# Kernel tuning notes

Hardware: AMD Instinct MI355X
Metric: run time of the kernel (lower is better)

Reference implementation:

```python
import jax, jax.numpy as jnp
import numpy as np

B, N_VIS, NUM_PATCHES = 8, 256, 1024
D_MODEL, PATCH = 512, 16
NUM_LAYERS, D_STATE, D_CONV, EXPAND = 4, 16, 4, 2
D_INNER = EXPAND * D_MODEL
DT_RANK = D_MODEL // 16  # ceil(d_model/16) = 32, standard Mamba
EPS = 1e-6


def setup_inputs() -> dict:
    key = jax.random.key(0)
    ks = jax.random.split(key, 20)
    s = 0.02
    inp = {
        "x_visible": jax.random.normal(ks[0], (B, N_VIS, D_MODEL), jnp.float32),
        "ids_visible": jnp.sort(jax.random.randint(ks[1], (B, N_VIS), 0, NUM_PATCHES), axis=-1),
        "mask_token": s * jax.random.normal(ks[2], (1, 1, D_MODEL), jnp.float32),
        "pos_embed": s * jax.random.normal(ks[3], (1, NUM_PATCHES, D_MODEL), jnp.float32),
        "in_proj_w": s * jax.random.normal(ks[4], (NUM_LAYERS, D_MODEL, 2 * D_INNER), jnp.float32),
        "conv_w": s * jax.random.normal(ks[5], (NUM_LAYERS, D_INNER, D_CONV), jnp.float32),
        "conv_b": jnp.zeros((NUM_LAYERS, D_INNER), jnp.float32),
        "x_proj_w": s * jax.random.normal(ks[6], (NUM_LAYERS, D_INNER, DT_RANK + 2 * D_STATE), jnp.float32),
        "dt_proj_w": s * jax.random.normal(ks[7], (NUM_LAYERS, DT_RANK, D_INNER), jnp.float32),
        "dt_proj_b": 0.1 * jax.random.uniform(ks[8], (NUM_LAYERS, D_INNER), jnp.float32),
        "A_log": jnp.broadcast_to(jnp.log(jnp.arange(1, D_STATE + 1, dtype=jnp.float32)), (NUM_LAYERS, D_INNER, D_STATE)) * jnp.ones((NUM_LAYERS, D_INNER, 1)),
        "D_skip": jnp.ones((NUM_LAYERS, D_INNER), jnp.float32),
        "out_proj_w": s * jax.random.normal(ks[9], (NUM_LAYERS, D_INNER, D_MODEL), jnp.float32),
        "block_norm_w": jnp.ones((NUM_LAYERS, D_MODEL), jnp.float32),
        "norm_w": jnp.ones((D_MODEL,), jnp.float32),
        "head_w": s * jax.random.normal(ks[10], (D_MODEL, PATCH), jnp.float32),
        "head_b": jnp.zeros((PATCH,), jnp.float32),
    }
    return inp


def rmsnorm(x, w):
    return x * jax.lax.rsqrt(jnp.mean(x * x, axis=-1, keepdims=True) + EPS) * w


def mamba_block(x, in_w, cw, cb, xp_w, dt_w, dt_b, a_log, d_skip, out_w):
    # x: [B, L, d_model]
    u, z = jnp.split(x @ in_w, 2, axis=-1)  # each [B, L, d_inner]
    # causal depthwise conv1d over L
    u_t = jnp.swapaxes(u, 1, 2)  # [B, d_inner, L]
    u_c = jax.lax.conv_general_dilated(
        u_t, cw[:, None, :], (1,), [(D_CONV - 1, 0)],
        dimension_numbers=("NCH", "OIH", "NCH"), feature_group_count=D_INNER)
    u = jax.nn.silu(jnp.swapaxes(u_c, 1, 2) + cb)  # [B, L, d_inner]
    x_dbl = u @ xp_w  # [B, L, dt_rank + 2*d_state]
    dt, Bm, Cm = jnp.split(x_dbl, [DT_RANK, DT_RANK + D_STATE], axis=-1)
    dt = jax.nn.softplus(dt @ dt_w + dt_b)  # [B, L, d_inner]
    A = -jnp.exp(a_log)  # [d_inner, d_state]

    def step(h, inp):
        dt_t, B_t, C_t, u_tt = inp  # [B,di], [B,ds], [B,ds], [B,di]
        dA = jnp.exp(dt_t[:, :, None] * A)  # [B, di, ds]
        h = dA * h + (dt_t * u_tt)[:, :, None] * B_t[:, None, :]
        y = jnp.einsum("bds,bs->bd", h, C_t)
        return h, y

    bsz = u.shape[0]
    h0 = jnp.zeros((bsz, D_INNER, D_STATE), x.dtype)
    xs = (jnp.swapaxes(dt, 0, 1), jnp.swapaxes(Bm, 0, 1),
          jnp.swapaxes(Cm, 0, 1), jnp.swapaxes(u, 0, 1))
    _, ys = jax.lax.scan(step, h0, xs)  # ys: [L, B, d_inner]
    y = jnp.swapaxes(ys, 0, 1) + u * d_skip
    y = y * jax.nn.silu(z)
    return y @ out_w


def reference(x_visible, ids_visible, mask_token, pos_embed, in_proj_w, conv_w,
              conv_b, x_proj_w, dt_proj_w, dt_proj_b, A_log, D_skip, out_proj_w,
              block_norm_w, norm_w, head_w, head_b):
    bsz = x_visible.shape[0]
    # scatter visible tokens into full mask-token canvas
    x_full = jnp.broadcast_to(mask_token, (bsz, NUM_PATCHES, D_MODEL))
    b_idx = jnp.arange(bsz)[:, None]
    x_full = x_full.at[b_idx, ids_visible].set(x_visible)
    x = x_full + pos_embed
    for i in range(NUM_LAYERS):
        x = x + mamba_block(rmsnorm(x, block_norm_w[i]), in_proj_w[i], conv_w[i],
                            conv_b[i], x_proj_w[i], dt_proj_w[i], dt_proj_b[i],
                            A_log[i], D_skip[i], out_proj_w[i])
    x = rmsnorm(x, norm_w)
    return x @ head_w + head_b
```

## Files before the change

### kernel.cpp

```cpp
#include <hip/hip_runtime.h>

typedef unsigned short u16;
typedef unsigned int   u32;
typedef __attribute__((ext_vector_type(8))) short bf16x8;
typedef __attribute__((ext_vector_type(4))) float f32x4;

__device__ __forceinline__ float b2f(u16 u) {
    union { u32 i; float f; } v; v.i = ((u32)u) << 16; return v.f;
}
__device__ __forceinline__ u16 f2b(float f) {
    union { float f; u32 i; } v; v.f = f;
    u32 x = v.i;
    return (u16)((x + 0x7fffu + ((x >> 16) & 1u)) >> 16);
}
__device__ __forceinline__ float ldf(const void* p, size_t i, int bf) {
    return bf ? b2f(((const u16*)p)[i]) : ((const float*)p)[i];
}

__global__ __launch_bounds__(256)
void prep_k(const void* __restrict__ alog, const void* __restrict__ dsk,
            const void* __restrict__ normw,
            float* __restrict__ a2f, float* __restrict__ df,
            int* __restrict__ flag)
{
    const int bf = (((const u16*)normw)[0] == 0x3F80u) ? 1 : 0;
    const int t = blockIdx.x * 256 + threadIdx.x;
    if (t == 0) { flag[0] = bf; flag[1] = 1; }
    const float v = -expf(ldf(alog, t, bf)) * 1.44269504f;
    a2f[t] = v;
    const float base = -expf(ldf(alog, t & ~15, bf)) * 1.44269504f;
    const float expect = (float)((t & 15) + 1) * base;
    if (fabsf(v - expect) > 1e-4f * fabsf(expect) + 1e-7f)
        atomicAnd(&flag[1], 0);
    if (t < 4096) df[t] = ldf(dsk, t, bf);
}

template<int BM, int EPI>
__global__ __launch_bounds__(256)
void gemm_gld_k(const u16* __restrict__ A, int lda,
                const u16* __restrict__ Bt, int K,
                float* __restrict__ C, int ldc,
                u16* __restrict__ C2)
{
    __shared__ __align__(16) u16 As[BM * 64];
    __shared__ __align__(16) u16 Bs[128 * 64];

    const int tid = threadIdx.x;
    const int NX = gridDim.x, NY = gridDim.y;
    const int bid = blockIdx.y * NX + blockIdx.x;
    const int xcd = bid & 7, j = bid >> 3;
    const int m_idx = xcd * (NY >> 3) + j / NX;
    const int n_idx = j % NX;
    const int m0 = m_idx * BM, n0 = n_idx * 128;

    const int lane = tid & 63, wave = tid >> 6;
    const int wr = wave >> 1, wc = wave & 1;
    constexpr int WM = BM / 2, FM = WM / 16;
    constexpr int AJ = BM / 32;

    const int lr = lane >> 3;
    const int skc = (lane & 7) ^ lr;

    f32x4 acc[FM][4] = {};

    for (int k0 = 0; k0 < K; k0 += 64) {
        #pragma unroll
        for (int j2 = 0; j2 < AJ; ++j2) {
            const int R = wave * (BM / 4) + j2 * 8;
            __builtin_amdgcn_global_load_lds(
                (const u32*)&A[(size_t)(m0 + R + lr) * lda + k0 + skc * 8],
                (u32*)&As[R * 64], 16, 0, 0);
        }
        #pragma unroll
        for (int j2 = 0; j2 < 4; ++j2) {
            const int R = wave * 32 + j2 * 8;
            __builtin_amdgcn_global_load_lds(
                (const u32*)&Bt[(size_t)(n0 + R + lr) * K + k0 + skc * 8],
                (u32*)&Bs[R * 64], 16, 0, 0);
        }
        __syncthreads();
        #pragma unroll
        for (int ks = 0; ks < 2; ++ks) {
            bf16x8 af[FM], bfr[4];
            const int chunk = ((ks * 4 + (lane >> 4)) ^ (lane & 7)) * 8;
            #pragma unroll
            for (int fm = 0; fm < FM; ++fm) {
                int m = wr * WM + fm * 16 + (lane & 15);
                af[fm] = *reinterpret_cast<const bf16x8*>(&As[m * 64 + chunk]);
            }
            #pragma unroll
            for (int fn = 0; fn < 4; ++fn) {
                int n = wc * 64 + fn * 16 + (lane & 15);
                bfr[fn] = *reinterpret_cast<const bf16x8*>(&Bs[n * 64 + chunk]);
            }
            #pragma unroll
            for (int fm = 0; fm < FM; ++fm)
                #pragma unroll
                for (int fn = 0; fn < 4; ++fn)
                    acc[fm][fn] = __builtin_amdgcn_mfma_f32_16x16x32_bf16(
                        af[fm], bfr[fn], acc[fm][fn], 0, 0, 0);
        }
        __syncthreads();
    }

    #pragma unroll
    for (int fm = 0; fm < FM; ++fm) {
        #pragma unroll
        for (int fn = 0; fn < 4; ++fn) {
            #pragma unroll
            for (int r = 0; r < 4; ++r) {
                int row = m0 + wr * WM + fm * 16 + ((lane >> 4) << 2) + r;
                int col = n0 + wc * 64 + fn * 16 + (lane & 15);
                float v = acc[fm][fn][r];
                size_t ci = (size_t)row * ldc + col;
                if constexpr (EPI == 0) C2[ci] = f2b(v);
                else                    C[ci] += v;
            }
        }
    }
}

template<int BM, int BN, int BK, int EPI, int SPLITK = 1, int AF32 = 0>
__global__ __launch_bounds__(256)
void gemm_k(const u16* __restrict__ A, int lda,
            const u16* __restrict__ Bt, int K,
            float* __restrict__ C, int ldc,
            u16* __restrict__ C2,
            const void* __restrict__ bias, int boff, const int* __restrict__ bff,
            int sstride = 0)
{
    constexpr int PAD = 8;
    constexpr int LDS_S = BK + PAD;
    __shared__ __align__(16) u16 As[BM * LDS_S];
    __shared__ __align__(16) u16 Bs[BN * LDS_S];

    const int tid = threadIdx.x;
    const int m0 = blockIdx.y * BM;
    int n0, kbeg, kend;
    if constexpr (SPLITK > 1) {
        n0 = 0;
        const int ksz = K / SPLITK;
        kbeg = blockIdx.x * ksz;
        kend = kbeg + ksz;
        C += (size_t)blockIdx.x * sstride;
    } else {
        n0 = blockIdx.x * BN;
        kbeg = 0; kend = K;
    }
    const int lane = tid & 63, wv = tid >> 6;
    const int wr = wv >> 1, wc = wv & 1;
    constexpr int WM = BM / 2, WN = BN / 2, FM = WM / 16, FN = WN / 16;
    constexpr int AC = (BM * BK) / 2048;
    constexpr int BC = (BN * BK) / 2048;
    constexpr int KC = BK / 8;

    f32x4 acc[FM][FN] = {};

    for (int k0 = kbeg; k0 < kend; k0 += BK) {
        #pragma unroll
        for (int i = 0; i < AC; ++i) {
            int idx = tid + i * 256;
            int row = idx / KC, kc = idx % KC;
            if constexpr (AF32) {
                const float* Af = (const float*)A;
                const float4 f0 = *reinterpret_cast<const float4*>(
                    &Af[(size_t)(m0 + row) * lda + k0 + kc * 8]);
                const float4 f1 = *reinterpret_cast<const float4*>(
                    &Af[(size_t)(m0 + row) * lda + k0 + kc * 8 + 4]);
                uint4 pk;
                pk.x = f2b(f0.x) | ((u32)f2b(f0.y) << 16);
                pk.y = f2b(f0.z) | ((u32)f2b(f0.w) << 16);
                pk.z = f2b(f1.x) | ((u32)f2b(f1.y) << 16);
                pk.w = f2b(f1.z) | ((u32)f2b(f1.w) << 16);
                *reinterpret_cast<uint4*>(&As[row * LDS_S + kc * 8]) = pk;
            } else {
                *reinterpret_cast<uint4*>(&As[row * LDS_S + kc * 8]) =
                    *reinterpret_cast<const uint4*>(&A[(size_t)(m0 + row) * lda + k0 + kc * 8]);
            }
        }
        #pragma unroll
        for (int i = 0; i < BC; ++i) {
            int idx = tid + i * 256;
            int row = idx / KC, kc = idx % KC;
            *reinterpret_cast<uint4*>(&Bs[row * LDS_S + kc * 8]) =
                *reinterpret_cast<const uint4*>(&Bt[(size_t)(n0 + row) * K + k0 + kc * 8]);
        }
        __syncthreads();
        #pragma unroll
        for (int ks = 0; ks < BK / 32; ++ks) {
            bf16x8 af[FM], bfr[FN];
            const int koff = ks * 32 + (lane >> 4) * 8;
            #pragma unroll
            for (int fm = 0; fm < FM; ++fm) {
                int m = wr * WM + fm * 16 + (lane & 15);
                af[fm] = *reinterpret_cast<const bf16x8*>(&As[m * LDS_S + koff]);
            }
            #pragma unroll
            for (int fn = 0; fn < FN; ++fn) {
                int n = wc * WN + fn * 16 + (lane & 15);
                bfr[fn] = *reinterpret_cast<const bf16x8*>(&Bs[n * LDS_S + koff]);
            }
            #pragma unroll
            for (int fm = 0; fm < FM; ++fm)
                #pragma unroll
                for (int fn = 0; fn < FN; ++fn)
                    acc[fm][fn] = __builtin_amdgcn_mfma_f32_16x16x32_bf16(
                        af[fm], bfr[fn], acc[fm][fn], 0, 0, 0);
        }
        __syncthreads();
    }

    int bf = 0;
    if constexpr (EPI == 2) bf = bff[0];

    #pragma unroll
    for (int fm = 0; fm < FM; ++fm) {
        #pragma unroll
        for (int fn = 0; fn < FN; ++fn) {
            #pragma unroll
            for (int r = 0; r < 4; ++r) {
                int row = m0 + wr * WM + fm * 16 + ((lane >> 4) << 2) + r;
                int col = n0 + wc * WN + fn * 16 + (lane & 15);
                float v = acc[fm][fn][r];
                size_t ci = (size_t)row * ldc + col;
                if constexpr (EPI == 2) {
                    v += ldf(bias, boff + col, bf);
                    v = (v > 20.f) ? v : __logf(1.f + __expf(v));
                    C2[ci] = f2b(v);
                } else {
                    C[ci] = v;
                }
            }
        }
    }
}

__global__ __launch_bounds__(256)
void xred_k(const float* __restrict__ xdp, float* __restrict__ xdf)
{
    const int t = blockIdx.x * 256 + threadIdx.x;
    constexpr int S = 8192 * 64;
    xdf[t] = (xdp[t] + xdp[t + S]) + (xdp[t + 2 * S] + xdp[t + 3 * S]);
}

__global__ __launch_bounds__(256)
void tr_k(const void* __restrict__ src, u16* __restrict__ dst, int K, int N,
          const int* __restrict__ bff)
{
    __shared__ u16 t[32][33];
    const int bf = bff[0];
    const size_t lo = (size_t)blockIdx.z * K * N;
    const int n0 = blockIdx.x * 32, k0 = blockIdx.y * 32;
    const int tx = threadIdx.x & 31, ty = threadIdx.x >> 5;
    #pragma unroll
    for (int q = 0; q < 4; ++q) {
        int r = ty + q * 8;
        size_t si = lo + (size_t)(k0 + r) * N + n0 + tx;
        t[r][tx] = bf ? ((const u16*)src)[si] : f2b(((const float*)src)[si]);
    }
    __syncthreads();
    #pragma unroll
    for (int q = 0; q < 4; ++q) {
        int r = ty + q * 8;
        dst[lo + (size_t)(n0 + r) * K + k0 + tx] = t[tx][r];
    }
}

__global__ __launch_bounds__(128)
void embed_k(const void* __restrict__ xv, const int* __restrict__ ids,
             const void* __restrict__ mtok, const void* __restrict__ pos,
             float* __restrict__ x, const int* __restrict__ bff)
{
    const int bf = bff[0];
    const int bid = blockIdx.x;
    const int p = bid & 1023, b = bid >> 10;
    const int* row = ids + b * 256;
    int lo = 0, hi = 256;
    while (lo < hi) { int mid = (lo + hi) >> 1; if (row[mid] <= p) lo = mid + 1; else hi = mid; }
    const int j = (lo > 0 && row[lo - 1] == p) ? (lo - 1) : -1;
    const int c = threadIdx.x * 4;
    const size_t sbase = (j >= 0) ? ((size_t)(b * 256 + j) * 512 + c) : (size_t)c;
    const void* srcp = (j >= 0) ? xv : mtok;
    const size_t o = (size_t)(b * 1024 + p) * 512 + c;
    #pragma unroll
    for (int e = 0; e < 4; ++e)
        x[o + e] = ldf(srcp, sbase + e, bf) + ldf(pos, (size_t)p * 512 + c + e, bf);
}

__global__ __launch_bounds__(128)
void rms_k(const float* __restrict__ x, const void* __restrict__ w, int wo,
           u16* __restrict__ xn, const int* __restrict__ bff)
{
    const int bf = bff[0];
    const int row = blockIdx.x, tid = threadIdx.x;
    const float4 v = *reinterpret_cast<const float4*>(&x[(size_t)row * 512 + tid * 4]);
    float ss = v.x * v.x + v.y * v.y + v.z * v.z + v.w * v.w;
    #pragma unroll
    for (int off = 32; off >= 1; off >>= 1) ss += __shfl_xor(ss, off);
    __shared__ float sred[2];
    if ((tid & 63) == 0) sred[tid >> 6] = ss;
    __syncthreads();
    const float scale = rsqrtf((sred[0] + sred[1]) * (1.f / 512.f) + 1e-6f);
    const int c = tid * 4;
    u32 plo = f2b(v.x * scale * ldf(w, wo + c + 0, bf)) | ((u32)f2b(v.y * scale * ldf(w, wo + c + 1, bf)) << 16);
    u32 phi = f2b(v.z * scale * ldf(w, wo + c + 2, bf)) | ((u32)f2b(v.w * scale * ldf(w, wo + c + 3, bf)) << 16);
    uint2 pk; pk.x = plo; pk.y = phi;
    *reinterpret_cast<uint2*>(&xn[(size_t)row * 512 + c]) = pk;
}

__global__ __launch_bounds__(256)
void conv_k(const u16* __restrict__ uz, const void* __restrict__ cw, int cwo,
            const void* __restrict__ cb, int cbo,
            u16* __restrict__ ucb, const int* __restrict__ bff)
{
    const int bf = bff[0];
    const int bid = blockIdx.x, tid = threadIdx.x;
    const int d = (bid & 3) * 256 + tid;
    const int lg = (bid >> 2) & 127;
    const int b = bid >> 9;
    const int l0 = lg * 8;
    const float w0 = ldf(cw, cwo + d * 4 + 0, bf), w1 = ldf(cw, cwo + d * 4 + 1, bf);
    const float w2 = ldf(cw, cwo + d * 4 + 2, bf), w3 = ldf(cw, cwo + d * 4 + 3, bf);
    const float bias = ldf(cb, cbo + d, bf);
    float u[11];
    #pragma unroll
    for (int j = 0; j < 11; ++j) {
        int l = l0 - 3 + j;
        u[j] = (l >= 0) ? b2f(uz[(size_t)(b * 1024 + l) * 2048 + d]) : 0.f;
    }
    #pragma unroll
    for (int i = 0; i < 8; ++i) {
        float a = bias + w0 * u[i] + w1 * u[i + 1] + w2 * u[i + 2] + w3 * u[i + 3];
        float s = a * (1.f / (1.f + __expf(-a)));
        ucb[(size_t)(b * 1024 + l0 + i) * 1024 + d] = f2b(s);
    }
}

__global__ __launch_bounds__(256)
void scan1_k(const u16* __restrict__ uz, const u16* __restrict__ ucb,
             const float* __restrict__ xdbl, const float* __restrict__ a2f, int alo,
             const float* __restrict__ df, int dso,
             u16* __restrict__ hcar, float* __restrict__ dtsum,
             u16* __restrict__ yloc, const int* __restrict__ astrp)
{
    const int tid = threadIdx.x;
    const int d = (blockIdx.x << 8) + tid;
    const int c = blockIdx.y, b = blockIdx.z;
    const int l0 = c * 16;
    const int astr = astrp[0];
    float h[16];
    #pragma unroll
    for (int s = 0; s < 16; ++s) h[s] = 0.f;
    const float* ap = &a2f[alo + d * 16];
    float A2[16];
    const float A2_0 = ap[0];
    if (!astr) {
        #pragma unroll
        for (int s = 0; s < 16; s += 4) {
            const float4 av = *reinterpret_cast<const float4*>(&ap[s]);
            A2[s] = av.x; A2[s+1] = av.y; A2[s+2] = av.z; A2[s+3] = av.w;
        }
    }
    const float Dv = df[dso + d];
    float dsum = 0.f;
    const u16* uzp = uz  + (size_t)(b * 1024 + l0) * 2048 + d;
    const u16* ucp = ucb + (size_t)(b * 1024 + l0) * 1024 + d;
    const float* xb = xdbl + (size_t)(b * 1024 + l0) * 64 + 32;
    u16* ylp = yloc + (size_t)(b * 1024 + l0) * 1024 + d;
    if (astr) {
        #pragma unroll 8
        for (int i = 0; i < 16; ++i) {
            float dtv = b2f(uzp[(size_t)i * 2048]);
            float uv  = b2f(ucp[(size_t)i * 1024]);
            float dtu = dtv * uv;
            dsum += dtv;
            const float4 B0 = *reinterpret_cast<const float4*>(xb + i * 64);
            const float4 B1 = *reinterpret_cast<const float4*>(xb + i * 64 + 4);
            const float4 B2 = *reinterpret_cast<const float4*>(xb + i * 64 + 8);
            const float4 B3 = *reinterpret_cast<const float4*>(xb + i * 64 + 12);
            const float4 C0 = *reinterpret_cast<const float4*>(xb + i * 64 + 16);
            const float4 C1 = *reinterpret_cast<const float4*>(xb + i * 64 + 20);
            const float4 C2 = *reinterpret_cast<const float4*>(xb + i * 64 + 24);
            const float4 C3 = *reinterpret_cast<const float4*>(xb + i * 64 + 28);
            const float Bv[16] = {B0.x,B0.y,B0.z,B0.w, B1.x,B1.y,B1.z,B1.w,
                                  B2.x,B2.y,B2.z,B2.w, B3.x,B3.y,B3.z,B3.w};
            const float Cv[16] = {C0.x,C0.y,C0.z,C0.w, C1.x,C1.y,C1.z,C1.w,
                                  C2.x,C2.y,C2.z,C2.w, C3.x,C3.y,C3.z,C3.w};
            float q  = exp2f(dtv * A2_0);
            float q2 = q * q, q3 = q2 * q, q4 = q2 * q2;
            float g1 = q, g2 = q2, g3 = q3, g4 = q4;
            float yv = 0.f;
            #pragma unroll
            for (int gr = 0; gr < 4; ++gr) {
                h[4*gr+0] = g1 * h[4*gr+0] + dtu * Bv[4*gr+0];
                h[4*gr+1] = g2 * h[4*gr+1] + dtu * Bv[4*gr+1];
                h[4*gr+2] = g3 * h[4*gr+2] + dtu * Bv[4*gr+2];
                h[4*gr+3] = g4 * h[4*gr+3] + dtu * Bv[4*gr+3];
                yv += h[4*gr+0] * Cv[4*gr+0] + h[4*gr+1] * Cv[4*gr+1]
                    + h[4*gr+2] * Cv[4*gr+2] + h[4*gr+3] * Cv[4*gr+3];
                if (gr < 3) { g1 *= q4; g2 *= q4; g3 *= q4; g4 *= q4; }
            }
            ylp[(size_t)i * 1024] = f2b(yv + uv * Dv);
        }
    } else {
        #pragma unroll 4
        for (int i = 0; i < 16; ++i) {
            float dtv = b2f(uzp[(size_t)i * 2048]);
            float uv  = b2f(ucp[(size_t)i * 1024]);
            float dtu = dtv * uv;
            dsum += dtv;
            const float4 B0 = *reinterpret_cast<const float4*>(xb + i * 64);
            const float4 B1 = *reinterpret_cast<const float4*>(xb + i * 64 + 4);
            const float4 B2 = *reinterpret_cast<const float4*>(xb + i * 64 + 8);
            const float4 B3 = *reinterpret_cast<const float4*>(xb + i * 64 + 12);
            const float4 C0 = *reinterpret_cast<const float4*>(xb + i * 64 + 16);
            const float4 C1 = *reinterpret_cast<const float4*>(xb + i * 64 + 20);
            const float4 C2 = *reinterpret_cast<const float4*>(xb + i * 64 + 24);
            const float4 C3 = *reinterpret_cast<const float4*>(xb + i * 64 + 28);
            const float Bv[16] = {B0.x,B0.y,B0.z,B0.w, B1.x,B1.y,B1.z,B1.w,
                                  B2.x,B2.y,B2.z,B2.w, B3.x,B3.y,B3.z,B3.w};
            const float Cv[16] = {C0.x,C0.y,C0.z,C0.w, C1.x,C1.y,C1.z,C1.w,
                                  C2.x,C2.y,C2.z,C2.w, C3.x,C3.y,C3.z,C3.w};
            float yv = 0.f;
            #pragma unroll
            for (int s = 0; s < 16; ++s) {
                h[s] = exp2f(dtv * A2[s]) * h[s] + dtu * Bv[s];
                yv += h[s] * Cv[s];
            }
            ylp[(size_t)i * 1024] = f2b(yv + uv * Dv);
        }
    }
    u16* hp = &hcar[((size_t)(b * 64 + c) * 1024 + d) * 16];
    #pragma unroll
    for (int s = 0; s < 16; s += 8) {
        uint4 pk;
        pk.x = f2b(h[s+0]) | ((u32)f2b(h[s+1]) << 16);
        pk.y = f2b(h[s+2]) | ((u32)f2b(h[s+3]) << 16);
        pk.z = f2b(h[s+4]) | ((u32)f2b(h[s+5]) << 16);
        pk.w = f2b(h[s+6]) | ((u32)f2b(h[s+7]) << 16);
        *reinterpret_cast<uint4*>(&hp[s]) = pk;
    }
    dtsum[(size_t)(b * 64 + c) * 1024 + d] = dsum;
}

__global__ __launch_bounds__(256)
void carry_k(u16* __restrict__ hcar, const float* __restrict__ dtsum,
             const float* __restrict__ a2f, int alo)
{
    const int t = blockIdx.x * 256 + threadIdx.x;
    const int b = t >> 14;
    const int ds = t & 16383;
    const int d = ds >> 4;
    const float A2 = a2f[alo + ds];
    float h = 0.f;
    #pragma unroll 8
    for (int c = 0; c < 64; ++c) {
        const size_t idx = (size_t)(b * 64 + c) * 16384 + ds;
        const float hl = b2f(hcar[idx]);
        hcar[idx] = f2b(h);
        h = exp2f(A2 * dtsum[(size_t)(b * 64 + c) * 1024 + d]) * h + hl;
    }
}

__global__ __launch_bounds__(256)
void scan2_k(const u16* __restrict__ uz, const u16* __restrict__ yloc,
             const float* __restrict__ xdbl, const float* __restrict__ a2f, int alo,
             const u16* __restrict__ hcar, u16* __restrict__ y,
             const int* __restrict__ astrp)
{
    const int tid = threadIdx.x;
    const int d = (blockIdx.x << 8) + tid;
    const int c = blockIdx.y, b = blockIdx.z;
    const int l0 = c * 16;
    const int astr = astrp[0];
    float hs[16];
    const float* ap = &a2f[alo + d * 16];
    const u16* hp = &hcar[(size_t)(b * 64 + c) * 16384 + d * 16];
    const float A2_0 = ap[0];
    float A2[16];
    if (!astr) {
        #pragma unroll
        for (int s = 0; s < 16; s += 4) {
            const float4 av = *reinterpret_cast<const float4*>(&ap[s]);
            A2[s] = av.x; A2[s+1] = av.y; A2[s+2] = av.z; A2[s+3] = av.w;
        }
    }
    #pragma unroll
    for (int s = 0; s < 16; s += 8) {
        const uint4 pk = *reinterpret_cast<const uint4*>(&hp[s]);
        hs[s+0] = b2f((u16)(pk.x & 0xffff)); hs[s+1] = b2f((u16)(pk.x >> 16));
        hs[s+2] = b2f((u16)(pk.y & 0xffff)); hs[s+3] = b2f((u16)(pk.y >> 16));
        hs[s+4] = b2f((u16)(pk.z & 0xffff)); hs[s+5] = b2f((u16)(pk.z >> 16));
        hs[s+6] = b2f((u16)(pk.w & 0xffff)); hs[s+7] = b2f((u16)(pk.w >> 16));
    }
    const u16* uzp = uz   + (size_t)(b * 1024 + l0) * 2048 + d;
    const u16* ylp = yloc + (size_t)(b * 1024 + l0) * 1024 + d;
    const float* xb = xdbl + (size_t)(b * 1024 + l0) * 64 + 48;
    u16* yp_ = y + (size_t)(b * 1024 + l0) * 1024 + d;
    float S = 0.f;
    if (astr) {
        #pragma unroll 8
        for (int i = 0; i < 16; ++i) {
            float dtv = b2f(uzp[(size_t)i * 2048]);
            float zv  = b2f(uzp[(size_t)i * 2048 + 1024]);
            float ylv = b2f(ylp[(size_t)i * 1024]);
            S += dtv;
            const float4 C0 = *reinterpret_cast<const float4*>(xb + i * 64);
            const float4 C1 = *reinterpret_cast<const float4*>(xb + i * 64 + 4);
            const float4 C2 = *reinterpret_cast<const float4*>(xb + i * 64 + 8);
            const float4 C3 = *reinterpret_cast<const float4*>(xb + i * 64 + 12);
            const float Cv[16] = {C0.x,C0.y,C0.z,C0.w, C1.x,C1.y,C1.z,C1.w,
                                  C2.x,C2.y,C2.z,C2.w, C3.x,C3.y,C3.z,C3.w};
            float q  = exp2f(S * A2_0);
            float q2 = q * q, q3 = q2 * q, q4 = q2 * q2;
            float g1 = q, g2 = q2, g3 = q3, g4 = q4;
            float corr = 0.f;
            #pragma unroll
            for (int gr = 0; gr < 4; ++gr) {
                corr += (g1 * hs[4*gr+0]) * Cv[4*gr+0] + (g2 * hs[4*gr+1]) * Cv[4*gr+1]
                      + (g3 * hs[4*gr+2]) * Cv[4*gr+2] + (g4 * hs[4*gr+3]) * Cv[4*gr+3];
                if (gr < 3) { g1 *= q4; g2 *= q4; g3 *= q4; g4 *= q4; }
            }
            float yo = (ylv + corr) * (zv * (1.f / (1.f + __expf(-zv))));
            yp_[(size_t)i * 1024] = f2b(yo);
        }
    } else {
        #pragma unroll 4
        for (int i = 0; i < 16; ++i) {
            float dtv = b2f(uzp[(size_t)i * 2048]);
            float zv  = b2f(uzp[(size_t)i * 2048 + 1024]);
            float ylv = b2f(ylp[(size_t)i * 1024]);
            S += dtv;
            const float4 C0 = *reinterpret_cast<const float4*>(xb + i * 64);
            const float4 C1 = *reinterpret_cast<const float4*>(xb + i * 64 + 4);
            const float4 C2 = *reinterpret_cast<const float4*>(xb + i * 64 + 8);
            const float4 C3 = *reinterpret_cast<const float4*>(xb + i * 64 + 12);
            const float Cv[16] = {C0.x,C0.y,C0.z,C0.w, C1.x,C1.y,C1.z,C1.w,
                                  C2.x,C2.y,C2.z,C2.w, C3.x,C3.y,C3.z,C3.w};
            float corr = 0.f;
            #pragma unroll
            for (int s = 0; s < 16; ++s)
                corr += (exp2f(S * A2[s]) * hs[s]) * Cv[s];
            float yo = (ylv + corr) * (zv * (1.f / (1.f + __expf(-zv))));
            yp_[(size_t)i * 1024] = f2b(yo);
        }
    }
}

__global__ __launch_bounds__(128)
void head_k(const float* __restrict__ x, const void* __restrict__ nw,
            const void* __restrict__ hw, const void* __restrict__ hb,
            void* __restrict__ out, const int* __restrict__ bff)
{
    const int bf = bff[0];
    const int row = blockIdx.x, tid = threadIdx.x;
    __shared__ float xs[512];
    __shared__ float pr[128];
    __shared__ float sred[2];
    const float4 v = *reinterpret_cast<const float4*>(&x[(size_t)row * 512 + tid * 4]);
    float ss = v.x * v.x + v.y * v.y + v.z * v.z + v.w * v.w;
    #pragma unroll
    for (int off = 32; off >= 1; off >>= 1) ss += __shfl_xor(ss, off);
    if ((tid & 63) == 0) sred[tid >> 6] = ss;
    __syncthreads();
    const float scale = rsqrtf((sred[0] + sred[1]) * (1.f / 512.f) + 1e-6f);
    const int c = tid * 4;
    xs[c + 0] = v.x * scale * ldf(nw, c + 0, bf);
    xs[c + 1] = v.y * scale * ldf(nw, c + 1, bf);
    xs[c + 2] = v.z * scale * ldf(nw, c + 2, bf);
    xs[c + 3] = v.w * scale * ldf(nw, c + 3, bf);
    __syncthreads();
    const int n = tid & 15, kg = tid >> 4;
    float s = 0.f;
    if (bf) {
        #pragma unroll 8
        for (int k = kg * 64; k < kg * 64 + 64; ++k)
            s += xs[k] * b2f(((const u16*)hw)[k * 16 + n]);
    } else {
        #pragma unroll 8
        for (int k = kg * 64; k < kg * 64 + 64; ++k)
            s += xs[k] * ((const float*)hw)[k * 16 + n];
    }
    pr[tid] = s;
    __syncthreads();
    if (tid < 16) {
        float a = ldf(hb, tid, bf);
        #pragma unroll
        for (int g = 0; g < 8; ++g) a += pr[g * 16 + tid];
        if (bf) ((u16*)out)[(size_t)row * 16 + tid] = f2b(a);
        else    ((float*)out)[(size_t)row * 16 + tid] = a;
    }
}

extern "C" void kernel_launch(void* const* d_in, const int* in_sizes, int n_in,
                              void* d_out, int out_size, void* d_ws, size_t ws_size,
                              hipStream_t stream)
{
    const void* xv   = d_in[0];
    const int*  ids  = (const int*)d_in[1];
    const void* mtok = d_in[2];
    const void* pos  = d_in[3];
    const void* inw  = d_in[4];
    const void* cw   = d_in[5];
    const void* cb   = d_in[6];
    const void* xpw  = d_in[7];
    const void* dtw  = d_in[8];
    const void* dtb  = d_in[9];
    const void* alog = d_in[10];
    const void* dsk  = d_in[11];
    const void* outw = d_in[12];
    const void* bnw  = d_in[13];
    const void* nw   = d_in[14];
    const void* hw   = d_in[15];
    const void* hb   = d_in[16];
    (void)in_sizes; (void)n_in; (void)out_size; (void)ws_size;

    char* base = (char*)d_ws;
    size_t off = 0;
    auto alloc = [&](size_t bytes) {
        char* p = base + off;
        off += (bytes + 255) & ~(size_t)255;
        return p;
    };
    int*   flag = (int*)  alloc(256);
    float* x    = (float*)alloc(8192ull * 512 * 4);
    u16*   xn   = (u16*)  alloc(8192ull * 512 * 2);
    u16*   uzb  = (u16*)  alloc(8192ull * 2048 * 2);
    u16*   ucb  = (u16*)  alloc(8192ull * 1024 * 2);
    float* xdf  = (float*)alloc(8192ull * 64 * 4);
    float* xdp  = (float*)alloc(4ull * 8192 * 64 * 4);
    u16*   yb   = (u16*)  alloc(8192ull * 1024 * 2);
    u16*   ylb  = (u16*)  alloc(8192ull * 1024 * 2);
    u16*   wTin = (u16*)  alloc(4ull * 2048 * 512 * 2);
    u16*   wTxp = (u16*)  alloc(4ull * 64 * 1024 * 2);
    u16*   wTdt = (u16*)  alloc(4ull * 1024 * 32 * 2);
    u16*   wTout= (u16*)  alloc(4ull * 512 * 1024 * 2);
    float* dtsum= (float*)alloc(8ull * 64 * 1024 * 4);
    u16*   hcar = (u16*)  alloc(8ull * 64 * 16384 * 2);
    float* a2f  = (float*)alloc(4ull * 16384 * 4);
    float* dff  = (float*)alloc(4ull * 1024 * 4);

    prep_k<<<256, 256, 0, stream>>>(alog, dsk, nw, a2f, dff, flag);

    tr_k<<<dim3(2048 / 32, 512 / 32, 4), 256, 0, stream>>>(inw, wTin, 512, 2048, flag);
    tr_k<<<dim3(64 / 32, 1024 / 32, 4), 256, 0, stream>>>(xpw, wTxp, 1024, 64, flag);
    tr_k<<<dim3(1024 / 32, 32 / 32, 4), 256, 0, stream>>>(dtw, wTdt, 32, 1024, flag);
    tr_k<<<dim3(512 / 32, 1024 / 32, 4), 256, 0, stream>>>(outw, wTout, 1024, 512, flag);

    embed_k<<<8192, 128, 0, stream>>>(xv, ids, mtok, pos, x, flag);

    for (int i = 0; i < 4; ++i) {
        rms_k<<<8192, 128, 0, stream>>>(x, bnw, i * 512, xn, flag);
        gemm_gld_k<128, 0><<<dim3(16, 64), 256, 0, stream>>>(
            xn, 512, wTin + (size_t)i * 2048 * 512, 512, nullptr, 2048, uzb);
        conv_k<<<4096, 256, 0, stream>>>(uzb, cw, i * 4096, cb, i * 1024, ucb, flag);
        gemm_k<64, 64, 64, 4, 4><<<dim3(4, 128), 256, 0, stream>>>(
            ucb, 1024, wTxp + (size_t)i * 64 * 1024, 1024, xdp, 64, nullptr,
            nullptr, 0, nullptr, 8192 * 64);
        xred_k<<<2048, 256, 0, stream>>>(xdp, xdf);
        gemm_k<64, 64, 32, 2, 1, 1><<<dim3(16, 128), 256, 0, stream>>>(
            (const u16*)xdf, 64, wTdt + (size_t)i * 1024 * 32, 32, nullptr, 2048, uzb,
            dtb, i * 1024, flag);
        scan1_k<<<dim3(4, 64, 8), 256, 0, stream>>>(
            uzb, ucb, xdf, a2f, i * 16384, dff, i * 1024, hcar, dtsum, ylb, flag + 1);
        carry_k<<<512, 256, 0, stream>>>(hcar, dtsum, a2f, i * 16384);
        scan2_k<<<dim3(4, 64, 8), 256, 0, stream>>>(
            uzb, ylb, xdf, a2f, i * 16384, hcar, yb, flag + 1);
        gemm_gld_k<64, 1><<<dim3(4, 128), 256, 0, stream>>>(
            yb, 1024, wTout + (size_t)i * 512 * 1024, 1024, x, 512, nullptr);
    }

    head_k<<<8192, 128, 0, stream>>>(x, nw, hw, hb, d_out, flag);
}
```

Before: 775.1 us.

## Fuse RMSNorm scaling into in-projection GEMM A-tile load

```diff
diff --git a/kernel.cpp b/kernel.cpp
--- a/kernel.cpp
+++ b/kernel.cpp
@@ -19,9 +19,9 @@
 
 __global__ __launch_bounds__(256)
 void prep_k(const void* __restrict__ alog, const void* __restrict__ dsk,
-            const void* __restrict__ normw,
+            const void* __restrict__ normw, const void* __restrict__ bnw,
             float* __restrict__ a2f, float* __restrict__ df,
-            int* __restrict__ flag)
+            float* __restrict__ bnwf, int* __restrict__ flag)
 {
     const int bf = (((const u16*)normw)[0] == 0x3F80u) ? 1 : 0;
     const int t = blockIdx.x * 256 + threadIdx.x;
@@ -33,14 +33,33 @@
     if (fabsf(v - expect) > 1e-4f * fabsf(expect) + 1e-7f)
         atomicAnd(&flag[1], 0);
     if (t < 4096) df[t] = ldf(dsk, t, bf);
-}
-
-template<int BM, int EPI>
+    if (t < 2048) bnwf[t] = ldf(bnw, t, bf);
+}
+
+__global__ __launch_bounds__(256)
+void rscale_k(const float* __restrict__ x, float* __restrict__ rs)
+{
+    const int wave = threadIdx.x >> 6, lane = threadIdx.x & 63;
+    const int row = blockIdx.x * 4 + wave;
+    const float* xp = x + (size_t)row * 512 + lane * 8;
+    const float4 v0 = *reinterpret_cast<const float4*>(xp);
+    const float4 v1 = *reinterpret_cast<const float4*>(xp + 4);
+    float ss = v0.x*v0.x + v0.y*v0.y + v0.z*v0.z + v0.w*v0.w
+             + v1.x*v1.x + v1.y*v1.y + v1.z*v1.z + v1.w*v1.w;
+    #pragma unroll
+    for (int off = 32; off >= 1; off >>= 1) ss += __shfl_xor(ss, off);
+    if (lane == 0) rs[row] = rsqrtf(ss * (1.f / 512.f) + 1e-6f);
+}
+
+template<int BM, int EPI, int ASCALE = 0>
 __global__ __launch_bounds__(256)
 void gemm_gld_k(const u16* __restrict__ A, int lda,
                 const u16* __restrict__ Bt, int K,
                 float* __restrict__ C, int ldc,
-                u16* __restrict__ C2)
+                u16* __restrict__ C2,
+                const float* __restrict__ Ax = nullptr,
+                const float* __restrict__ rs = nullptr,
+                const float* __restrict__ wn = nullptr)
 {
     __shared__ __align__(16) u16 As[BM * 64];
     __shared__ __align__(16) u16 Bs[128 * 64];
@@ -64,12 +83,34 @@
     f32x4 acc[FM][4] = {};
 
     for (int k0 = 0; k0 < K; k0 += 64) {
-        #pragma unroll
-        for (int j2 = 0; j2 < AJ; ++j2) {
-            const int R = wave * (BM / 4) + j2 * 8;
-            __builtin_amdgcn_global_load_lds(
-                (const u32*)&A[(size_t)(m0 + R + lr) * lda + k0 + skc * 8],
-                (u32*)&As[R * 64], 16, 0, 0);
+        if constexpr (ASCALE) {
+            constexpr int AC = (BM * 64) / 2048;
+            #pragma unroll
+            for (int i = 0; i < AC; ++i) {
+                const int idx = tid + i * 256;
+                const int row = idx >> 3, kc = idx & 7;
+                const float rsv = rs[m0 + row];
+                const float* xp = Ax + (size_t)(m0 + row) * lda + k0 + kc * 8;
+                const float* wp = wn + k0 + kc * 8;
+                const float4 f0 = *reinterpret_cast<const float4*>(xp);
+                const float4 f1 = *reinterpret_cast<const float4*>(xp + 4);
+                const float4 w0 = *reinterpret_cast<const float4*>(wp);
+                const float4 w1 = *reinterpret_cast<const float4*>(wp + 4);
+                uint4 pk;
+                pk.x = f2b(f0.x * rsv * w0.x) | ((u32)f2b(f0.y * rsv * w0.y) << 16);
+                pk.y = f2b(f0.z * rsv * w0.z) | ((u32)f2b(f0.w * rsv * w0.w) << 16);
+                pk.z = f2b(f1.x * rsv * w1.x) | ((u32)f2b(f1.y * rsv * w1.y) << 16);
+                pk.w = f2b(f1.z * rsv * w1.z) | ((u32)f2b(f1.w * rsv * w1.w) << 16);
+                *reinterpret_cast<uint4*>(&As[row * 64 + (kc ^ (row & 7)) * 8]) = pk;
+            }
+        } else {
+            #pragma unroll
+            for (int j2 = 0; j2 < AJ; ++j2) {
+                const int R = wave * (BM / 4) + j2 * 8;
+                __builtin_amdgcn_global_load_lds(
+                    (const u32*)&A[(size_t)(m0 + R + lr) * lda + k0 + skc * 8],
+                    (u32*)&As[R * 64], 16, 0, 0);
+            }
         }
         #pragma unroll
         for (int j2 = 0; j2 < 4; ++j2) {
@@ -161,7 +202,7 @@
         for (int i = 0; i < AC; ++i) {
             int idx = tid + i * 256;
             int row = idx / KC, kc = idx % KC;
-            if constexpr (AF32) {
+            if constexpr (AF32 == 1) {
                 const float* Af = (const float*)A;
                 const float4 f0 = *reinterpret_cast<const float4*>(
                     &Af[(size_t)(m0 + row) * lda + k0 + kc * 8]);
@@ -285,27 +326,6 @@
     #pragma unroll
     for (int e = 0; e < 4; ++e)
         x[o + e] = ldf(srcp, sbase + e, bf) + ldf(pos, (size_t)p * 512 + c + e, bf);
-}
-
-__global__ __launch_bounds__(128)
-void rms_k(const float* __restrict__ x, const void* __restrict__ w, int wo,
-           u16* __restrict__ xn, const int* __restrict__ bff)
-{
-    const int bf = bff[0];
-    const int row = blockIdx.x, tid = threadIdx.x;
-    const float4 v = *reinterpret_cast<const float4*>(&x[(size_t)row * 512 + tid * 4]);
-    float ss = v.x * v.x + v.y * v.y + v.z * v.z + v.w * v.w;
-    #pragma unroll
-    for (int off = 32; off >= 1; off >>= 1) ss += __shfl_xor(ss, off);
-    __shared__ float sred[2];
-    if ((tid & 63) == 0) sred[tid >> 6] = ss;
-    __syncthreads();
-    const float scale = rsqrtf((sred[0] + sred[1]) * (1.f / 512.f) + 1e-6f);
-    const int c = tid * 4;
-    u32 plo = f2b(v.x * scale * ldf(w, wo + c + 0, bf)) | ((u32)f2b(v.y * scale * ldf(w, wo + c + 1, bf)) << 16);
-    u32 phi = f2b(v.z * scale * ldf(w, wo + c + 2, bf)) | ((u32)f2b(v.w * scale * ldf(w, wo + c + 3, bf)) << 16);
-    uint2 pk; pk.x = plo; pk.y = phi;
-    *reinterpret_cast<uint2*>(&xn[(size_t)row * 512 + c]) = pk;
 }
 
 __global__ __launch_bounds__(256)
@@ -624,7 +644,7 @@
     };
     int*   flag = (int*)  alloc(256);
     float* x    = (float*)alloc(8192ull * 512 * 4);
-    u16*   xn   = (u16*)  alloc(8192ull * 512 * 2);
+    float* rsb  = (float*)alloc(8192ull * 4);
     u16*   uzb  = (u16*)  alloc(8192ull * 2048 * 2);
     u16*   ucb  = (u16*)  alloc(8192ull * 1024 * 2);
     float* xdf  = (float*)alloc(8192ull * 64 * 4);
@@ -639,8 +659,9 @@
     u16*   hcar = (u16*)  alloc(8ull * 64 * 16384 * 2);
     float* a2f  = (float*)alloc(4ull * 16384 * 4);
     float* dff  = (float*)alloc(4ull * 1024 * 4);
-
-    prep_k<<<256, 256, 0, stream>>>(alog, dsk, nw, a2f, dff, flag);
+    float* bnwf = (float*)alloc(4ull * 512 * 4);
+
+    prep_k<<<256, 256, 0, stream>>>(alog, dsk, nw, bnw, a2f, dff, bnwf, flag);
 
     tr_k<<<dim3(2048 / 32, 512 / 32, 4), 256, 0, stream>>>(inw, wTin, 512, 2048, flag);
     tr_k<<<dim3(64 / 32, 1024 / 32, 4), 256, 0, stream>>>(xpw, wTxp, 1024, 64, flag);
@@ -650,9 +671,10 @@
     embed_k<<<8192, 128, 0, stream>>>(xv, ids, mtok, pos, x, flag);
 
     for (int i = 0; i < 4; ++i) {
-        rms_k<<<8192, 128, 0, stream>>>(x, bnw, i * 512, xn, flag);
-        gemm_gld_k<128, 0><<<dim3(16, 64), 256, 0, stream>>>(
-            xn, 512, wTin + (size_t)i * 2048 * 512, 512, nullptr, 2048, uzb);
+        rscale_k<<<2048, 256, 0, stream>>>(x, rsb);
+        gemm_gld_k<128, 0, 1><<<dim3(16, 64), 256, 0, stream>>>(
+            nullptr, 512, wTin + (size_t)i * 2048 * 512, 512, nullptr, 2048, uzb,
+            x, rsb, bnwf + i * 512);
         conv_k<<<4096, 256, 0, stream>>>(uzb, cw, i * 4096, cb, i * 1024, ucb, flag);
         gemm_k<64, 64, 64, 4, 4><<<dim3(4, 128), 256, 0, stream>>>(
             ucb, 1024, wTxp + (size_t)i * 64 * 1024, 1024, xdp, 64, nullptr,
```

Result: slower. 796.6 us (+2.8%).
